# Optimization experiments

Measured on AMD Instinct MI355X. Metric: run time of the kernel, lower is better.

Reference implementation:

```python
import jax, jax.numpy as jnp
import numpy as np

NUM_HEADS = 8
LN_EPS = 1e-5


def _comm_matrix(E):
    # chain graph: connection (i, i+1) with weight 0.5, symmetric
    cm = jnp.zeros((E, E), dtype=jnp.float32)
    idx = jnp.arange(E - 1)
    cm = cm.at[idx, idx + 1].set(0.5)
    return cm + cm.T


def setup_inputs() -> dict:
    key = jax.random.key(0)
    B, E, H = 2048, 16, 1024
    ks = jax.random.split(key, 8)
    s = 0.02
    return {
        "x": jax.random.normal(ks[0], (B, E, H), dtype=jnp.float32),
        "ln_g": jnp.ones((H,), jnp.float32),
        "ln_b": jnp.zeros((H,), jnp.float32),
        "wq": jax.random.normal(ks[1], (H, H), jnp.float32) * s,
        "bq": jnp.zeros((H,), jnp.float32),
        "wk": jax.random.normal(ks[2], (H, H), jnp.float32) * s,
        "bk": jnp.zeros((H,), jnp.float32),
        "wv": jax.random.normal(ks[3], (H, H), jnp.float32) * s,
        "bv": jnp.zeros((H,), jnp.float32),
        "wo": jax.random.normal(ks[4], (H, H), jnp.float32) * s,
        "bo": jnp.zeros((H,), jnp.float32),
        "wg": jax.random.normal(ks[5], (1, 2 * H), jnp.float32) * s,
        "bg": jnp.zeros((1,), jnp.float32),
    }


def reference(x, ln_g, ln_b, wq, bq, wk, bk, wv, bv, wo, bo, wg, bg):
    B, E, H = x.shape
    nh = NUM_HEADS
    hd = H // nh

    # --- graph communication: comm_matrix @ x over expert dim ---
    cm = _comm_matrix(E)                              # [E, E]
    comm = jnp.einsum('ef,bfh->beh', cm, x)           # [B, E, H]

    # --- cross-attention block (pre-LN, residual) ---
    residual = comm
    mu = comm.mean(-1, keepdims=True)
    var = comm.var(-1, keepdims=True)
    xn = (comm - mu) * jax.lax.rsqrt(var + LN_EPS) * ln_g + ln_b

    q = (xn @ wq.T + bq).reshape(B, E, nh, hd)
    k = (xn @ wk.T + bk).reshape(B, E, nh, hd)
    v = (xn @ wv.T + bv).reshape(B, E, nh, hd)

    scores = jnp.einsum('bqnd,bknd->bnqk', q, k) / (hd ** 0.5)  # [B, nh, E, E]
    attn = jax.nn.softmax(scores, axis=-1)
    attended = jnp.einsum('bnqk,bknd->bqnd', attn, v).reshape(B, E, H)
    comm_out = attended @ wo.T + bo + residual        # [B, E, H]

    # --- communication gate ---
    gate_in = jnp.concatenate([x, comm_out], axis=-1)  # [B, E, 2H]
    gate = jax.nn.sigmoid(gate_in @ wg.T + bg)         # [B, E, 1]
    return gate * comm_out + (1.0 - gate) * x
```

## Files before the change

### kernel.cpp

```cpp
#include <hip/hip_runtime.h>
#include <cstdint>
#include <cstddef>

#define HDIM 1024
#define EEXP 16
#define BATCH 2048
#define MROWS (BATCH * EEXP)
#define NHEADS 8
#define HEADD 128
#define KDIM 1024
#define LN_EPS 1e-5f

typedef __bf16 bf16x8_t __attribute__((ext_vector_type(8)));
typedef float f32x4_t __attribute__((ext_vector_type(4)));
typedef unsigned short u16x4_t __attribute__((ext_vector_type(4)));
typedef unsigned short u16x8_t __attribute__((ext_vector_type(8)));

__device__ __forceinline__ unsigned short f2bf(float f) {
    unsigned int u = __builtin_bit_cast(unsigned int, f);
    unsigned int r = (u + 0x7FFFu + ((u >> 16) & 1u)) >> 16;
    return (unsigned short)r;
}
__device__ __forceinline__ float bf2f(unsigned short h) {
    unsigned int u = ((unsigned int)h) << 16;
    return __builtin_bit_cast(float, u);
}

__global__ __launch_bounds__(256) void k_conv4(
    const float* __restrict__ s0, const float* __restrict__ s1,
    const float* __restrict__ s2, const float* __restrict__ s3,
    unsigned short* __restrict__ d0, unsigned short* __restrict__ d1,
    unsigned short* __restrict__ d2, unsigned short* __restrict__ d3) {
    const int which = blockIdx.x >> 10;
    const int i = ((blockIdx.x & 1023) * 256 + threadIdx.x) * 4;
    const float* s = (which == 0) ? s0 : (which == 1) ? s1 : (which == 2) ? s2 : s3;
    unsigned short* d = (which == 0) ? d0 : (which == 1) ? d1 : (which == 2) ? d2 : d3;
    float4 v = *(const float4*)(s + i);
    u16x4_t o;
    o.x = f2bf(v.x); o.y = f2bf(v.y); o.z = f2bf(v.z); o.w = f2bf(v.w);
    *(u16x4_t*)(d + i) = o;
}

__global__ __launch_bounds__(256) void k_prep(const float* __restrict__ x,
                                              const float* __restrict__ lng,
                                              const float* __restrict__ lnb,
                                              unsigned short* __restrict__ xn) {
    const int m = blockIdx.x;
    const int e = m & (EEXP - 1);
    const int t = threadIdx.x;
    const int h = t * 4;
    const float* xr = x + (size_t)m * HDIM;

    float c0 = 0.f, c1 = 0.f, c2 = 0.f, c3 = 0.f;
    if (e > 0) {
        float4 v = *(const float4*)(xr - HDIM + h);
        c0 = 0.5f * v.x; c1 = 0.5f * v.y; c2 = 0.5f * v.z; c3 = 0.5f * v.w;
    }
    if (e < EEXP - 1) {
        float4 v = *(const float4*)(xr + HDIM + h);
        c0 += 0.5f * v.x; c1 += 0.5f * v.y; c2 += 0.5f * v.z; c3 += 0.5f * v.w;
    }
    float s  = c0 + c1 + c2 + c3;
    float ss = c0 * c0 + c1 * c1 + c2 * c2 + c3 * c3;
#pragma unroll
    for (int off = 32; off; off >>= 1) {
        s  += __shfl_xor(s, off, 64);
        ss += __shfl_xor(ss, off, 64);
    }
    __shared__ float red[8];
    const int wv = t >> 6;
    if ((t & 63) == 0) { red[wv] = s; red[4 + wv] = ss; }
    __syncthreads();
    s  = red[0] + red[1] + red[2] + red[3];
    ss = red[4] + red[5] + red[6] + red[7];
    const float mean = s * (1.0f / HDIM);
    const float var  = ss * (1.0f / HDIM) - mean * mean;
    const float rinv = rsqrtf(var + LN_EPS);

    float4 g = *(const float4*)(lng + h);
    float4 b = *(const float4*)(lnb + h);
    u16x4_t o;
    o.x = f2bf((c0 - mean) * rinv * g.x + b.x);
    o.y = f2bf((c1 - mean) * rinv * g.y + b.y);
    o.z = f2bf((c2 - mean) * rinv * g.z + b.z);
    o.w = f2bf((c3 - mean) * rinv * g.w + b.w);
    *(u16x4_t*)(xn + (size_t)m * HDIM + h) = o;
}

template <int N, bool IS_QKV>
__global__ __launch_bounds__(256) void k_gemm(
    const unsigned short* __restrict__ A,
    const unsigned short* __restrict__ Bw,
    const float* __restrict__ b0,
    const float* __restrict__ b1,
    const float* __restrict__ b2,
    unsigned short* __restrict__ Cbf,
    float* __restrict__ Cf) {
    constexpr int K = KDIM;
    constexpr int NTILES = N / 128;
    __shared__ unsigned short As[128 * 32];
    __shared__ unsigned short Bs[128 * 32];

    const int tid  = threadIdx.x;
    const int nt   = blockIdx.x % NTILES;
    const int mt   = blockIdx.x / NTILES;
    const int m0   = mt * 128, n0 = nt * 128;
    const int lane = tid & 63, wave = tid >> 6;
    const int wm   = (wave >> 1) * 64, wn = (wave & 1) * 64;
    const int quad = lane >> 4, r16 = lane & 15;
    const int srow = tid >> 2;
    const int skk  = (((tid & 3) ^ ((srow >> 1) & 3)) * 8);
    const int slot = (quad ^ ((r16 >> 1) & 3)) * 8;

    f32x4_t acc[4][4];
#pragma unroll
    for (int i = 0; i < 4; i++)
#pragma unroll
        for (int j = 0; j < 4; j++) acc[i][j] = f32x4_t{0.f, 0.f, 0.f, 0.f};

    const unsigned short* Ag = A + (size_t)(m0 + srow) * K + skk;
    const unsigned short* Bg = Bw + (size_t)(n0 + srow) * K + skk;

    for (int k0 = 0; k0 < K; k0 += 32) {
        __syncthreads();
        __builtin_amdgcn_global_load_lds(
            (const __attribute__((address_space(1))) void*)(Ag + k0),
            (__attribute__((address_space(3))) void*)(As + tid * 8), 16, 0, 0);
        __builtin_amdgcn_global_load_lds(
            (const __attribute__((address_space(1))) void*)(Ag + (size_t)64 * K + k0),
            (__attribute__((address_space(3))) void*)(As + 2048 + tid * 8), 16, 0, 0);
        __builtin_amdgcn_global_load_lds(
            (const __attribute__((address_space(1))) void*)(Bg + k0),
            (__attribute__((address_space(3))) void*)(Bs + tid * 8), 16, 0, 0);
        __builtin_amdgcn_global_load_lds(
            (const __attribute__((address_space(1))) void*)(Bg + (size_t)64 * K + k0),
            (__attribute__((address_space(3))) void*)(Bs + 2048 + tid * 8), 16, 0, 0);
        __syncthreads();

        bf16x8_t a[4], b[4];
#pragma unroll
        for (int i = 0; i < 4; i++)
            a[i] = *(const bf16x8_t*)&As[(wm + i * 16 + r16) * 32 + slot];
#pragma unroll
        for (int j = 0; j < 4; j++)
            b[j] = *(const bf16x8_t*)&Bs[(wn + j * 16 + r16) * 32 + slot];
#pragma unroll
        for (int i = 0; i < 4; i++)
#pragma unroll
            for (int j = 0; j < 4; j++)
                acc[i][j] = __builtin_amdgcn_mfma_f32_16x16x32_bf16(b[j], a[i], acc[i][j], 0, 0, 0);
    }

    float4 bias4[4];
#pragma unroll
    for (int j = 0; j < 4; j++) {
        const int col0 = n0 + wn + j * 16 + quad * 4;
        if constexpr (IS_QKV) {
            const float* bp = (col0 < 1024) ? (b0 + col0)
                             : (col0 < 2048) ? (b1 + col0 - 1024)
                                             : (b2 + col0 - 2048);
            bias4[j] = *(const float4*)bp;
        } else {
            bias4[j] = *(const float4*)(b0 + col0);
        }
    }
#pragma unroll
    for (int i = 0; i < 4; i++) {
        const int grow = m0 + wm + i * 16 + r16;
#pragma unroll
        for (int j = 0; j < 4; j++) {
            const int col0 = n0 + wn + j * 16 + quad * 4;
            if constexpr (IS_QKV) {
                u16x4_t o;
                o.x = f2bf(acc[i][j][0] + bias4[j].x);
                o.y = f2bf(acc[i][j][1] + bias4[j].y);
                o.z = f2bf(acc[i][j][2] + bias4[j].z);
                o.w = f2bf(acc[i][j][3] + bias4[j].w);
                *(u16x4_t*)&Cbf[(size_t)grow * N + col0] = o;
            } else {
                float4 o;
                o.x = acc[i][j][0] + bias4[j].x;
                o.y = acc[i][j][1] + bias4[j].y;
                o.z = acc[i][j][2] + bias4[j].z;
                o.w = acc[i][j][3] + bias4[j].w;
                *(float4*)&Cf[(size_t)grow * N + col0] = o;
            }
        }
    }
}

__global__ __launch_bounds__(256) void k_attn(const unsigned short* __restrict__ qkv,
                                              unsigned short* __restrict__ att) {
    const int bidx = blockIdx.x;
    const int b = bidx >> 3, n = bidx & 7;
    __shared__ float qs[16][132], ks[16][132], vs[16][132];
    __shared__ float ps[16][17];
    const int t = threadIdx.x;

    {
        const int row = t >> 4, c0 = (t & 15) * 8;
        const size_t base = (size_t)(b * EEXP + row) * (3 * HDIM) + n * HEADD + c0;
        u16x8_t qv = *(const u16x8_t*)&qkv[base];
        u16x8_t kv = *(const u16x8_t*)&qkv[base + HDIM];
        u16x8_t vv = *(const u16x8_t*)&qkv[base + 2 * HDIM];
#pragma unroll
        for (int u = 0; u < 8; u++) {
            qs[row][c0 + u] = bf2f(qv[u]);
            ks[row][c0 + u] = bf2f(kv[u]);
            vs[row][c0 + u] = bf2f(vv[u]);
        }
    }
    __syncthreads();

    const int qe = t >> 4, ke = t & 15;
    float s = 0.f;
#pragma unroll 8
    for (int d = 0; d < HEADD; d += 4) {
        s += qs[qe][d] * ks[ke][d] + qs[qe][d + 1] * ks[ke][d + 1] +
             qs[qe][d + 2] * ks[ke][d + 2] + qs[qe][d + 3] * ks[ke][d + 3];
    }
    s *= 0.08838834764831845f;
    float mx = s;
#pragma unroll
    for (int off = 8; off; off >>= 1) mx = fmaxf(mx, __shfl_xor(mx, off, 16));
    const float ex = __expf(s - mx);
    float sum = ex;
#pragma unroll
    for (int off = 8; off; off >>= 1) sum += __shfl_xor(sum, off, 16);
    ps[qe][ke] = ex / sum;
    __syncthreads();

    const int dd = t & 15;
    float o[8] = {0.f, 0.f, 0.f, 0.f, 0.f, 0.f, 0.f, 0.f};
#pragma unroll
    for (int k2 = 0; k2 < EEXP; k2++) {
        const float p = ps[qe][k2];
#pragma unroll
        for (int u = 0; u < 8; u++) o[u] += p * vs[k2][dd + 16 * u];
    }
    const size_t ob = (size_t)(b * EEXP + qe) * HDIM + n * HEADD + dd;
#pragma unroll
    for (int u = 0; u < 8; u++) att[ob + 16 * u] = f2bf(o[u]);
}

__global__ __launch_bounds__(256) void k_gate(const float* __restrict__ x,
                                              const float* __restrict__ wg,
                                              const float* __restrict__ bg,
                                              float* __restrict__ out) {
    const int m = blockIdx.x;
    const int e = m & (EEXP - 1);
    const int t = threadIdx.x;
    const int h = t * 4;
    const float* xr = x + (size_t)m * HDIM;
    float* orow = out + (size_t)m * HDIM;

    float4 xv = *(const float4*)(xr + h);
    float4 rv = *(const float4*)(orow + h);
    float c0 = 0.f, c1 = 0.f, c2 = 0.f, c3 = 0.f;
    if (e > 0) {
        float4 v = *(const float4*)(xr - HDIM + h);
        c0 = 0.5f * v.x; c1 = 0.5f * v.y; c2 = 0.5f * v.z; c3 = 0.5f * v.w;
    }
    if (e < EEXP - 1) {
        float4 v = *(const float4*)(xr + HDIM + h);
        c0 += 0.5f * v.x; c1 += 0.5f * v.y; c2 += 0.5f * v.z; c3 += 0.5f * v.w;
    }
    const float co0 = rv.x + c0, co1 = rv.y + c1, co2 = rv.z + c2, co3 = rv.w + c3;

    float4 w1 = *(const float4*)(wg + h);
    float4 w2 = *(const float4*)(wg + HDIM + h);
    float d = xv.x * w1.x + xv.y * w1.y + xv.z * w1.z + xv.w * w1.w +
              co0 * w2.x + co1 * w2.y + co2 * w2.z + co3 * w2.w;
#pragma unroll
    for (int off = 32; off; off >>= 1) d += __shfl_xor(d, off, 64);
    __shared__ float red[4];
    const int wv = t >> 6;
    if ((t & 63) == 0) red[wv] = d;
    __syncthreads();
    const float tot = red[0] + red[1] + red[2] + red[3] + bg[0];
    const float gate = 1.0f / (1.0f + __expf(-tot));

    float4 ov;
    ov.x = gate * co0 + (1.0f - gate) * xv.x;
    ov.y = gate * co1 + (1.0f - gate) * xv.y;
    ov.z = gate * co2 + (1.0f - gate) * xv.z;
    ov.w = gate * co3 + (1.0f - gate) * xv.w;
    *(float4*)(orow + h) = ov;
}

extern "C" void kernel_launch(void* const* d_in, const int* in_sizes, int n_in,
                              void* d_out, int out_size, void* d_ws, size_t ws_size,
                              hipStream_t stream) {
    const float* x   = (const float*)d_in[0];
    const float* lng = (const float*)d_in[1];
    const float* lnb = (const float*)d_in[2];
    const float* wq  = (const float*)d_in[3];
    const float* bq  = (const float*)d_in[4];
    const float* wk  = (const float*)d_in[5];
    const float* bk  = (const float*)d_in[6];
    const float* wv  = (const float*)d_in[7];
    const float* bv  = (const float*)d_in[8];
    const float* wo  = (const float*)d_in[9];
    const float* bo  = (const float*)d_in[10];
    const float* wg  = (const float*)d_in[11];
    const float* bg  = (const float*)d_in[12];
    float* out = (float*)d_out;

    unsigned short* wqkv = (unsigned short*)d_ws;
    unsigned short* wob  = wqkv + (size_t)3072 * 1024;
    unsigned short* xn   = wob + (size_t)1024 * 1024;
    unsigned short* qkv  = xn + (size_t)MROWS * HDIM;
    unsigned short* att  = qkv + (size_t)MROWS * 3 * HDIM;

    const int WELTS = 1024 * 1024;
    k_conv4<<<4096, 256, 0, stream>>>(wq, wk, wv, wo,
                                      wqkv, wqkv + (size_t)WELTS,
                                      wqkv + (size_t)2 * WELTS, wob);

    k_prep<<<MROWS, 256, 0, stream>>>(x, lng, lnb, xn);

    k_gemm<3072, true><<<(MROWS / 128) * (3072 / 128), 256, 0, stream>>>(
        xn, wqkv, bq, bk, bv, qkv, nullptr);

    k_attn<<<BATCH * NHEADS, 256, 0, stream>>>(qkv, att);

    k_gemm<1024, false><<<(MROWS / 128) * (1024 / 128), 256, 0, stream>>>(
        att, wob, bo, nullptr, nullptr, nullptr, out);

    k_gate<<<MROWS, 256, 0, stream>>>(x, wg, bg, out);
}
```

Baseline: 817.1 us.

## Deepen GEMM K-tile to 64 with XCD-aware tile mapping; vectorize attention LDS

```diff
diff --git a/kernel.cpp b/kernel.cpp
--- a/kernel.cpp
+++ b/kernel.cpp
@@ -97,20 +97,29 @@
     unsigned short* __restrict__ Cbf,
     float* __restrict__ Cf) {
     constexpr int K = KDIM;
-    constexpr int NTILES = N / 128;
-    __shared__ unsigned short As[128 * 32];
-    __shared__ unsigned short Bs[128 * 32];
-
-    const int tid  = threadIdx.x;
-    const int nt   = blockIdx.x % NTILES;
-    const int mt   = blockIdx.x / NTILES;
-    const int m0   = mt * 128, n0 = nt * 128;
+    __shared__ unsigned short As[128 * 64];
+    __shared__ unsigned short Bs[128 * 64];
+
+    const int tid = threadIdx.x;
+    const int xcd = blockIdx.x & 7;
+    const int g   = blockIdx.x >> 3;
+    int mt, nt;
+    if constexpr (N == 3072) {
+        const int st = g / 96, r = g % 96;
+        mt = xcd * 32 + (st >> 1) * 8 + (r & 7);
+        nt = (st & 1) * 12 + (r >> 3);
+    } else {
+        const int st = g >> 6, r = g & 63;
+        mt = xcd * 32 + st * 8 + (r & 7);
+        nt = r >> 3;
+    }
+    const int m0 = mt * 128, n0 = nt * 128;
+
     const int lane = tid & 63, wave = tid >> 6;
     const int wm   = (wave >> 1) * 64, wn = (wave & 1) * 64;
     const int quad = lane >> 4, r16 = lane & 15;
-    const int srow = tid >> 2;
-    const int skk  = (((tid & 3) ^ ((srow >> 1) & 3)) * 8);
-    const int slot = (quad ^ ((r16 >> 1) & 3)) * 8;
+    const int srow = tid >> 3;
+    const int sgk  = ((tid & 7) ^ (srow & 7)) * 8;
 
     f32x4_t acc[4][4];
 #pragma unroll
@@ -118,52 +127,60 @@
 #pragma unroll
         for (int j = 0; j < 4; j++) acc[i][j] = f32x4_t{0.f, 0.f, 0.f, 0.f};
 
-    const unsigned short* Ag = A + (size_t)(m0 + srow) * K + skk;
-    const unsigned short* Bg = Bw + (size_t)(n0 + srow) * K + skk;
-
-    for (int k0 = 0; k0 < K; k0 += 32) {
-        __syncthreads();
-        __builtin_amdgcn_global_load_lds(
-            (const __attribute__((address_space(1))) void*)(Ag + k0),
-            (__attribute__((address_space(3))) void*)(As + tid * 8), 16, 0, 0);
-        __builtin_amdgcn_global_load_lds(
-            (const __attribute__((address_space(1))) void*)(Ag + (size_t)64 * K + k0),
-            (__attribute__((address_space(3))) void*)(As + 2048 + tid * 8), 16, 0, 0);
-        __builtin_amdgcn_global_load_lds(
-            (const __attribute__((address_space(1))) void*)(Bg + k0),
-            (__attribute__((address_space(3))) void*)(Bs + tid * 8), 16, 0, 0);
-        __builtin_amdgcn_global_load_lds(
-            (const __attribute__((address_space(1))) void*)(Bg + (size_t)64 * K + k0),
-            (__attribute__((address_space(3))) void*)(Bs + 2048 + tid * 8), 16, 0, 0);
-        __syncthreads();
-
-        bf16x8_t a[4], b[4];
-#pragma unroll
-        for (int i = 0; i < 4; i++)
-            a[i] = *(const bf16x8_t*)&As[(wm + i * 16 + r16) * 32 + slot];
-#pragma unroll
-        for (int j = 0; j < 4; j++)
-            b[j] = *(const bf16x8_t*)&Bs[(wn + j * 16 + r16) * 32 + slot];
-#pragma unroll
-        for (int i = 0; i < 4; i++)
-#pragma unroll
-            for (int j = 0; j < 4; j++)
-                acc[i][j] = __builtin_amdgcn_mfma_f32_16x16x32_bf16(b[j], a[i], acc[i][j], 0, 0, 0);
-    }
-
-    float4 bias4[4];
+    f32x4_t bias4[4];
 #pragma unroll
     for (int j = 0; j < 4; j++) {
         const int col0 = n0 + wn + j * 16 + quad * 4;
+        const float* bp;
         if constexpr (IS_QKV) {
-            const float* bp = (col0 < 1024) ? (b0 + col0)
-                             : (col0 < 2048) ? (b1 + col0 - 1024)
-                                             : (b2 + col0 - 2048);
-            bias4[j] = *(const float4*)bp;
+            bp = (col0 < 1024) ? (b0 + col0)
+               : (col0 < 2048) ? (b1 + col0 - 1024)
+                               : (b2 + col0 - 2048);
         } else {
-            bias4[j] = *(const float4*)(b0 + col0);
-        }
-    }
+            bp = b0 + col0;
+        }
+        bias4[j] = *(const f32x4_t*)bp;
+    }
+
+    const unsigned short* Ag = A + (size_t)(m0 + srow) * K + sgk;
+    const unsigned short* Bg = Bw + (size_t)(n0 + srow) * K + sgk;
+    const int swz0 = ((0 * 4 + quad) ^ (r16 & 7)) * 8;
+    const int swz1 = ((1 * 4 + quad) ^ (r16 & 7)) * 8;
+
+    for (int k0 = 0; k0 < K; k0 += 64) {
+        __syncthreads();
+#pragma unroll
+        for (int q = 0; q < 4; q++) {
+            __builtin_amdgcn_global_load_lds(
+                (const __attribute__((address_space(1))) void*)(Ag + (size_t)(q * 32) * K + k0),
+                (__attribute__((address_space(3))) void*)(As + q * 2048 + tid * 8), 16, 0, 0);
+        }
+#pragma unroll
+        for (int q = 0; q < 4; q++) {
+            __builtin_amdgcn_global_load_lds(
+                (const __attribute__((address_space(1))) void*)(Bg + (size_t)(q * 32) * K + k0),
+                (__attribute__((address_space(3))) void*)(Bs + q * 2048 + tid * 8), 16, 0, 0);
+        }
+        __syncthreads();
+
+#pragma unroll
+        for (int h = 0; h < 2; h++) {
+            const int swz = h ? swz1 : swz0;
+            bf16x8_t a[4], b[4];
+#pragma unroll
+            for (int i = 0; i < 4; i++)
+                a[i] = *(const bf16x8_t*)&As[(wm + i * 16 + r16) * 64 + swz];
+#pragma unroll
+            for (int j = 0; j < 4; j++)
+                b[j] = *(const bf16x8_t*)&Bs[(wn + j * 16 + r16) * 64 + swz];
+#pragma unroll
+            for (int i = 0; i < 4; i++)
+#pragma unroll
+                for (int j = 0; j < 4; j++)
+                    acc[i][j] = __builtin_amdgcn_mfma_f32_16x16x32_bf16(b[j], a[i], acc[i][j], 0, 0, 0);
+        }
+    }
+
 #pragma unroll
     for (int i = 0; i < 4; i++) {
         const int grow = m0 + wm + i * 16 + r16;
@@ -172,18 +189,18 @@
             const int col0 = n0 + wn + j * 16 + quad * 4;
             if constexpr (IS_QKV) {
                 u16x4_t o;
-                o.x = f2bf(acc[i][j][0] + bias4[j].x);
-                o.y = f2bf(acc[i][j][1] + bias4[j].y);
-                o.z = f2bf(acc[i][j][2] + bias4[j].z);
-                o.w = f2bf(acc[i][j][3] + bias4[j].w);
+                o.x = f2bf(acc[i][j][0] + bias4[j][0]);
+                o.y = f2bf(acc[i][j][1] + bias4[j][1]);
+                o.z = f2bf(acc[i][j][2] + bias4[j][2]);
+                o.w = f2bf(acc[i][j][3] + bias4[j][3]);
                 *(u16x4_t*)&Cbf[(size_t)grow * N + col0] = o;
             } else {
-                float4 o;
-                o.x = acc[i][j][0] + bias4[j].x;
-                o.y = acc[i][j][1] + bias4[j].y;
-                o.z = acc[i][j][2] + bias4[j].z;
-                o.w = acc[i][j][3] + bias4[j].w;
-                *(float4*)&Cf[(size_t)grow * N + col0] = o;
+                f32x4_t o;
+                o[0] = acc[i][j][0] + bias4[j][0];
+                o[1] = acc[i][j][1] + bias4[j][1];
+                o[2] = acc[i][j][2] + bias4[j][2];
+                o[3] = acc[i][j][3] + bias4[j][3];
+                *(f32x4_t*)&Cf[(size_t)grow * N + col0] = o;
             }
         }
     }
@@ -203,21 +220,26 @@
         u16x8_t qv = *(const u16x8_t*)&qkv[base];
         u16x8_t kv = *(const u16x8_t*)&qkv[base + HDIM];
         u16x8_t vv = *(const u16x8_t*)&qkv[base + 2 * HDIM];
-#pragma unroll
-        for (int u = 0; u < 8; u++) {
-            qs[row][c0 + u] = bf2f(qv[u]);
-            ks[row][c0 + u] = bf2f(kv[u]);
-            vs[row][c0 + u] = bf2f(vv[u]);
-        }
+        f32x4_t q0, q1, k0, k1, v0, v1;
+#pragma unroll
+        for (int u = 0; u < 4; u++) {
+            q0[u] = bf2f(qv[u]); q1[u] = bf2f(qv[u + 4]);
+            k0[u] = bf2f(kv[u]); k1[u] = bf2f(kv[u + 4]);
+            v0[u] = bf2f(vv[u]); v1[u] = bf2f(vv[u + 4]);
+        }
+        *(f32x4_t*)&qs[row][c0] = q0; *(f32x4_t*)&qs[row][c0 + 4] = q1;
+        *(f32x4_t*)&ks[row][c0] = k0; *(f32x4_t*)&ks[row][c0 + 4] = k1;
+        *(f32x4_t*)&vs[row][c0] = v0; *(f32x4_t*)&vs[row][c0 + 4] = v1;
     }
     __syncthreads();
 
     const int qe = t >> 4, ke = t & 15;
     float s = 0.f;
-#pragma unroll 8
+#pragma unroll
     for (int d = 0; d < HEADD; d += 4) {
-        s += qs[qe][d] * ks[ke][d] + qs[qe][d + 1] * ks[ke][d + 1] +
-             qs[qe][d + 2] * ks[ke][d + 2] + qs[qe][d + 3] * ks[ke][d + 3];
+        f32x4_t qv = *(const f32x4_t*)&qs[qe][d];
+        f32x4_t kv = *(const f32x4_t*)&ks[ke][d];
+        s += qv[0] * kv[0] + qv[1] * kv[1] + qv[2] * kv[2] + qv[3] * kv[3];
     }
     s *= 0.08838834764831845f;
     float mx = s;
@@ -230,17 +252,20 @@
     ps[qe][ke] = ex / sum;
     __syncthreads();
 
-    const int dd = t & 15;
+    const int dd8 = (t & 15) * 8;
     float o[8] = {0.f, 0.f, 0.f, 0.f, 0.f, 0.f, 0.f, 0.f};
 #pragma unroll
     for (int k2 = 0; k2 < EEXP; k2++) {
         const float p = ps[qe][k2];
-#pragma unroll
-        for (int u = 0; u < 8; u++) o[u] += p * vs[k2][dd + 16 * u];
-    }
-    const size_t ob = (size_t)(b * EEXP + qe) * HDIM + n * HEADD + dd;
-#pragma unroll
-    for (int u = 0; u < 8; u++) att[ob + 16 * u] = f2bf(o[u]);
+        f32x4_t v0 = *(const f32x4_t*)&vs[k2][dd8];
+        f32x4_t v1 = *(const f32x4_t*)&vs[k2][dd8 + 4];
+        o[0] += p * v0[0]; o[1] += p * v0[1]; o[2] += p * v0[2]; o[3] += p * v0[3];
+        o[4] += p * v1[0]; o[5] += p * v1[1]; o[6] += p * v1[2]; o[7] += p * v1[3];
+    }
+    u16x8_t ov;
+#pragma unroll
+    for (int u = 0; u < 8; u++) ov[u] = f2bf(o[u]);
+    *(u16x8_t*)&att[(size_t)(b * EEXP + qe) * HDIM + n * HEADD + dd8] = ov;
 }
 
 __global__ __launch_bounds__(256) void k_gate(const float* __restrict__ x,
```

Measured after the change: 797.2 us. 1.02x faster.
